# Optimization experiments

Measured on AMD Instinct MI355X. Metric: run time of the kernel, lower is better.

The kernel has to match this reference:

```python
import jax, jax.numpy as jnp
import numpy as np

IN_F = 128
OUT_F = 64


def _xavier(key, shape, gain=1.414):
    fan_in, fan_out = shape[0], shape[1]
    bound = gain * np.sqrt(6.0 / (fan_in + fan_out))
    return jax.random.uniform(key, shape, jnp.float32, -bound, bound)


def setup_inputs() -> dict:
    key = jax.random.key(0)
    ks = jax.random.split(key, 11)
    features = jax.random.normal(ks[0], (2, 32, 2048, IN_F), dtype=jnp.float32)
    d = {"features": features}
    for i in range(4):
        d[f"W{i+1}"] = _xavier(ks[1 + 2 * i], (IN_F, 2 * OUT_F))
        d[f"a{i+1}"] = _xavier(ks[2 + 2 * i], (2 * OUT_F, 1))
    d["Wo"] = _xavier(ks[9], (8 * OUT_F, OUT_F))
    return d


def _head(features, W, a):
    # features: [b,g,n,i]; W: [i,j]; a: [j,1]
    Wx = jnp.einsum('bgni,ij->bgnj', features, W)          # [b,g,n,2F]
    att = jax.nn.softmax(Wx @ a, axis=2)                   # softmax over nodes, [b,g,n,1]
    return jnp.einsum('bgno,bgnj->bgj', att, Wx)           # pooled [b,g,2F]


def reference(features, W1, a1, W2, a2, W3, a3, W4, a4, Wo):
    h1 = _head(features, W1, a1)
    h2 = _head(features, W2, a2)
    h3 = _head(features, W3, a3)
    h4 = _head(features, W4, a4)
    multi = jnp.concatenate([h1, h2, h3, h4], axis=2)      # [b,g,8F]
    return jax.nn.elu(multi @ Wo)                          # [b,g,F]
```

## Files before the change

### kernel.cpp

```cpp
#include <hip/hip_runtime.h>
#include <math.h>

#define BG     64
#define NN     2048
#define F      128
#define OUTF   64
#define NSLICE 32
#define SNODES 64

#define OFF_WEFF 0
#define OFF_FP   512
#define OFF_LP   (512 + BG * NSLICE * 4 * F)

__global__ __launch_bounds__(256) void k_weff(
    const float* __restrict__ W1, const float* __restrict__ a1,
    const float* __restrict__ W2, const float* __restrict__ a2,
    const float* __restrict__ W3, const float* __restrict__ a3,
    const float* __restrict__ W4, const float* __restrict__ a4,
    float* __restrict__ ws) {
  int h = blockIdx.x, t = threadIdx.x;
  const float* W = (h == 0) ? W1 : (h == 1) ? W2 : (h == 2) ? W3 : W4;
  const float* a = (h == 0) ? a1 : (h == 1) ? a2 : (h == 2) ? a3 : a4;
  __shared__ float aL[F];
  __shared__ float part[F][33];

  if (t < F) aL[t] = a[t];
  __syncthreads();

  int c = t & 31, r8 = t >> 5;
#pragma unroll
  for (int it = 0; it < 16; ++it) {
    int row = it * 8 + r8;
    float4 w = ((const float4*)(W + row * F))[c];
    part[row][c] = w.x * aL[4 * c] + w.y * aL[4 * c + 1] +
                   w.z * aL[4 * c + 2] + w.w * aL[4 * c + 3];
  }
  __syncthreads();

  if (t < F) {
    float s = 0.f;
#pragma unroll
    for (int c2 = 0; c2 < 32; ++c2) s += part[t][c2];
    ws[OFF_WEFF + h * F + t] = s;
  }
}

__global__ __launch_bounds__(256) void k_main(
    const float* __restrict__ feat, float* __restrict__ ws) {
  int g = blockIdx.x >> 5;
  int slice = blockIdx.x & (NSLICE - 1);
  int t = threadIdx.x;

  __shared__ float4 sfeat[SNODES * 32];
  __shared__ float4 weffL[4 * 32];
  __shared__ float eLf[SNODES * 4];
  __shared__ float4 pacc[4][2][32];
  __shared__ float sePf[2][4];

  if (t < 128) weffL[t] = ((const float4*)(ws + OFF_WEFF))[t];

  const float4* fb =
      (const float4*)(feat + ((size_t)g * NN + slice * SNODES) * F);
  float4 ld[8];
#pragma unroll
  for (int k = 0; k < 8; ++k) ld[k] = fb[k * 256 + t];
#pragma unroll
  for (int k = 0; k < 8; ++k) {
    int j = k * 256 + t;
    int n = j >> 5, c = j & 31;
    sfeat[n * 32 + (c ^ (n & 31))] = ld[k];
  }
  __syncthreads();

  {
    int n = t & 63, h = t >> 6;
    int sw = n & 31, base = n * 32, wb = h * 32;
    float p = 0.f;
#pragma unroll 8
    for (int c = 0; c < 32; ++c) {
      float4 f = sfeat[base + (c ^ sw)];
      float4 w = weffL[wb + c];
      p += f.x * w.x + f.y * w.y + f.z * w.z + f.w * w.w;
    }
    eLf[n * 4 + h] = __expf(p);
  }
  __syncthreads();

  {
    int i4 = t & 31, q = (t >> 5) & 1, h = t >> 6;
    float4 a0 = make_float4(0.f, 0.f, 0.f, 0.f);
    float se = 0.f;
#pragma unroll 8
    for (int nn = 0; nn < 32; ++nn) {
      int n = q * 32 + nn;
      float4 f = sfeat[n * 32 + (i4 ^ (n & 31))];
      float e = eLf[n * 4 + h];
      a0.x += e * f.x; a0.y += e * f.y; a0.z += e * f.z; a0.w += e * f.w;
      se += e;
    }
    pacc[h][q][i4] = a0;
    if (i4 == 0) sePf[q][h] = se;
  }
  __syncthreads();

  if (t < 128) {
    int i4 = t & 31, h = t >> 5;
    float4 s0 = pacc[h][0][i4], s1 = pacc[h][1][i4];
    float4 s = make_float4(s0.x + s1.x, s0.y + s1.y,
                           s0.z + s1.z, s0.w + s1.w);
    ((float4*)(ws + OFF_FP))[(size_t)(g * NSLICE + slice) * 128 + h * 32 + i4] = s;
  }
  if (t == 0) {
    float4 L = make_float4(sePf[0][0] + sePf[1][0], sePf[0][1] + sePf[1][1],
                           sePf[0][2] + sePf[1][2], sePf[0][3] + sePf[1][3]);
    ((float4*)(ws + OFF_LP))[g * NSLICE + slice] = L;
  }
}

__global__ __launch_bounds__(512) void k_final(
    const float* __restrict__ W1, const float* __restrict__ W2,
    const float* __restrict__ W3, const float* __restrict__ W4,
    const float* __restrict__ Wo, const float* __restrict__ ws,
    float* __restrict__ out) {
  int g = blockIdx.x;
  int t = threadIdx.x;
  __shared__ float fp[512];
  __shared__ float multi[512];
  __shared__ float invl[4];
  __shared__ float part[8][64];

  if (t < 4) {
    float s = 0.f;
#pragma unroll
    for (int sl = 0; sl < NSLICE; ++sl)
      s += ws[OFF_LP + (g * NSLICE + sl) * 4 + t];
    invl[t] = 1.0f / s;
  }
  float s = 0.f;
  const float* fpb = ws + OFF_FP + (size_t)g * NSLICE * 512 + t;
#pragma unroll
  for (int sl = 0; sl < NSLICE; ++sl) s += fpb[sl * 512];
  __syncthreads();
  fp[t] = s * invl[t >> 7];
  __syncthreads();

  int h = t >> 7, col = t & 127;
  const float* W = (h == 0) ? W1 : (h == 1) ? W2 : (h == 2) ? W3 : W4;
  const float* fph = fp + h * F;
  float acc = 0.f;
#pragma unroll 16
  for (int i = 0; i < F; ++i) acc += fph[i] * W[i * F + col];
  multi[t] = acc;
  __syncthreads();

  int o = t & 63, chunk = t >> 6;
  const float* mk = multi + chunk * 64;
  const float* wk = Wo + (size_t)chunk * 64 * OUTF + o;
  float p = 0.f;
#pragma unroll 16
  for (int k = 0; k < 64; ++k) p += mk[k] * wk[k * OUTF];
  part[chunk][o] = p;
  __syncthreads();

  if (t < 64) {
    float acc2 = 0.f;
#pragma unroll
    for (int c = 0; c < 8; ++c) acc2 += part[c][t];
    out[g * OUTF + t] = (acc2 > 0.f) ? acc2 : expm1f(acc2);
  }
}

extern "C" void kernel_launch(void* const* d_in, const int* in_sizes, int n_in,
                              void* d_out, int out_size, void* d_ws, size_t ws_size,
                              hipStream_t stream) {
  const float* feat = (const float*)d_in[0];
  const float* W1 = (const float*)d_in[1];
  const float* a1 = (const float*)d_in[2];
  const float* W2 = (const float*)d_in[3];
  const float* a2 = (const float*)d_in[4];
  const float* W3 = (const float*)d_in[5];
  const float* a3 = (const float*)d_in[6];
  const float* W4 = (const float*)d_in[7];
  const float* a4 = (const float*)d_in[8];
  const float* Wo = (const float*)d_in[9];
  float* ws = (float*)d_ws;
  float* out = (float*)d_out;

  k_weff<<<4, 256, 0, stream>>>(W1, a1, W2, a2, W3, a3, W4, a4, ws);
  k_main<<<BG * NSLICE, 256, 0, stream>>>(feat, ws);
  k_final<<<BG, 512, 0, stream>>>(W1, W2, W3, W4, Wo, ws, out);
}
```

Measured before the change: 119.2 us.

## Fuse final projection into main kernel via last-block atomic counter

Removes the separate k_final launch. Each k_main block bumps an atomic counter for its graph, and the last slice block to finish does the cross-slice reduction, the per-head W projection and the Wo projection with ELU. The final stage now uses float4 weight loads and split-K partial sums held in reused shared memory. This saves a kernel launch and its dependency gap, at the cost of threadfences, an atomic per block, and a serialized tail done by 64 blocks of 256 threads. It also sets launch_bounds occupancy to 4 blocks per SIMD-group.

```diff
diff --git a/kernel.cpp b/kernel.cpp
--- a/kernel.cpp
+++ b/kernel.cpp
@@ -9,8 +9,9 @@
 #define SNODES 64
 
 #define OFF_WEFF 0
-#define OFF_FP   512
-#define OFF_LP   (512 + BG * NSLICE * 4 * F)
+#define OFF_CNT  512
+#define OFF_FP   576
+#define OFF_LP   (576 + BG * NSLICE * 4 * F)
 
 __global__ __launch_bounds__(256) void k_weff(
     const float* __restrict__ W1, const float* __restrict__ a1,
@@ -24,6 +25,8 @@
   __shared__ float aL[F];
   __shared__ float part[F][33];
 
+  if (h == 0 && t < BG) ((int*)(ws + OFF_CNT))[t] = 0;
+
   if (t < F) aL[t] = a[t];
   __syncthreads();
 
@@ -45,8 +48,12 @@
   }
 }
 
-__global__ __launch_bounds__(256) void k_main(
-    const float* __restrict__ feat, float* __restrict__ ws) {
+__global__ __launch_bounds__(256, 4) void k_main(
+    const float* __restrict__ feat,
+    const float* __restrict__ W1, const float* __restrict__ W2,
+    const float* __restrict__ W3, const float* __restrict__ W4,
+    const float* __restrict__ Wo,
+    float* __restrict__ ws, float* __restrict__ out) {
   int g = blockIdx.x >> 5;
   int slice = blockIdx.x & (NSLICE - 1);
   int t = threadIdx.x;
@@ -56,6 +63,7 @@
   __shared__ float eLf[SNODES * 4];
   __shared__ float4 pacc[4][2][32];
   __shared__ float sePf[2][4];
+  __shared__ int lastFlag;
 
   if (t < 128) weffL[t] = ((const float4*)(ws + OFF_WEFF))[t];
 
@@ -115,58 +123,92 @@
                            sePf[0][2] + sePf[1][2], sePf[0][3] + sePf[1][3]);
     ((float4*)(ws + OFF_LP))[g * NSLICE + slice] = L;
   }
-}
-
-__global__ __launch_bounds__(512) void k_final(
-    const float* __restrict__ W1, const float* __restrict__ W2,
-    const float* __restrict__ W3, const float* __restrict__ W4,
-    const float* __restrict__ Wo, const float* __restrict__ ws,
-    float* __restrict__ out) {
-  int g = blockIdx.x;
-  int t = threadIdx.x;
-  __shared__ float fp[512];
-  __shared__ float multi[512];
-  __shared__ float invl[4];
-  __shared__ float part[8][64];
+
+  __threadfence();
+  __syncthreads();
+  if (t == 0) {
+    int old = atomicAdd((int*)(ws + OFF_CNT) + g, 1);
+    lastFlag = (old == NSLICE - 1) ? 1 : 0;
+  }
+  __syncthreads();
+  if (!lastFlag) return;
+  __threadfence();
+
+  float* fbuf = (float*)sfeat;
+  float4* f4 = (float4*)sfeat;
+  const float4* FP4 = (const float4*)(ws + OFF_FP) + (size_t)g * NSLICE * 128;
 
   if (t < 4) {
     float s = 0.f;
 #pragma unroll
     for (int sl = 0; sl < NSLICE; ++sl)
       s += ws[OFF_LP + (g * NSLICE + sl) * 4 + t];
-    invl[t] = 1.0f / s;
-  }
-  float s = 0.f;
-  const float* fpb = ws + OFF_FP + (size_t)g * NSLICE * 512 + t;
-#pragma unroll
-  for (int sl = 0; sl < NSLICE; ++sl) s += fpb[sl * 512];
-  __syncthreads();
-  fp[t] = s * invl[t >> 7];
-  __syncthreads();
-
-  int h = t >> 7, col = t & 127;
-  const float* W = (h == 0) ? W1 : (h == 1) ? W2 : (h == 2) ? W3 : W4;
-  const float* fph = fp + h * F;
-  float acc = 0.f;
-#pragma unroll 16
-  for (int i = 0; i < F; ++i) acc += fph[i] * W[i * F + col];
-  multi[t] = acc;
-  __syncthreads();
-
-  int o = t & 63, chunk = t >> 6;
-  const float* mk = multi + chunk * 64;
-  const float* wk = Wo + (size_t)chunk * 64 * OUTF + o;
-  float p = 0.f;
-#pragma unroll 16
-  for (int k = 0; k < 64; ++k) p += mk[k] * wk[k * OUTF];
-  part[chunk][o] = p;
-  __syncthreads();
-
-  if (t < 64) {
-    float acc2 = 0.f;
-#pragma unroll
-    for (int c = 0; c < 8; ++c) acc2 += part[c][t];
-    out[g * OUTF + t] = (acc2 > 0.f) ? acc2 : expm1f(acc2);
+    fbuf[8188 + t] = 1.0f / s;
+  }
+  {
+    int j = t & 127, half = t >> 7;
+    float4 s4 = make_float4(0.f, 0.f, 0.f, 0.f);
+#pragma unroll
+    for (int sl = 0; sl < 16; ++sl) {
+      float4 v = FP4[(half * 16 + sl) * 128 + j];
+      s4.x += v.x; s4.y += v.y; s4.z += v.z; s4.w += v.w;
+    }
+    f4[half * 128 + j] = s4;
+  }
+  __syncthreads();
+  if (t < 128) {
+    float4 a = f4[t], b = f4[128 + t];
+    float inv = fbuf[8188 + (t >> 5)];
+    f4[256 + t] = make_float4((a.x + b.x) * inv, (a.y + b.y) * inv,
+                              (a.z + b.z) * inv, (a.w + b.w) * inv);
+  }
+  __syncthreads();
+
+  {
+    int c = t & 31, rg = (t >> 5) & 1, h = t >> 6;
+    const float* Wsel = (h == 0) ? W1 : (h == 1) ? W2 : (h == 2) ? W3 : W4;
+    const float4* W4p = (const float4*)Wsel;
+    const float* fph = fbuf + 1024 + h * F;
+    float4 acc = make_float4(0.f, 0.f, 0.f, 0.f);
+#pragma unroll 8
+    for (int k = 0; k < 64; ++k) {
+      int i = rg * 64 + k;
+      float s = fph[i];
+      float4 w = W4p[i * 32 + c];
+      acc.x += s * w.x; acc.y += s * w.y; acc.z += s * w.z; acc.w += s * w.w;
+    }
+    f4[512 + (h * 2 + rg) * 32 + c] = acc;
+  }
+  __syncthreads();
+  if (t < 128) {
+    int h = t >> 5, c = t & 31;
+    float4 a = f4[512 + (h * 2) * 32 + c];
+    float4 b = f4[512 + (h * 2 + 1) * 32 + c];
+    f4[768 + h * 32 + c] = make_float4(a.x + b.x, a.y + b.y,
+                                       a.z + b.z, a.w + b.w);
+  }
+  __syncthreads();
+
+  {
+    int o4 = t & 15, rg = t >> 4;
+    const float4* Wo4 = (const float4*)Wo;
+    const float* mu = fbuf + 3072;
+    float4 acc = make_float4(0.f, 0.f, 0.f, 0.f);
+#pragma unroll 8
+    for (int k = 0; k < 32; ++k) {
+      int i = rg * 32 + k;
+      float s = mu[i];
+      float4 w = Wo4[i * 16 + o4];
+      acc.x += s * w.x; acc.y += s * w.y; acc.z += s * w.z; acc.w += s * w.w;
+    }
+    f4[rg * 16 + o4] = acc;
+  }
+  __syncthreads();
+  if (t < OUTF) {
+    float s = 0.f;
+#pragma unroll
+    for (int rg = 0; rg < 16; ++rg) s += fbuf[rg * 64 + t];
+    out[g * OUTF + t] = (s > 0.f) ? s : expm1f(s);
   }
 }
 
@@ -187,6 +229,5 @@
   float* out = (float*)d_out;
 
   k_weff<<<4, 256, 0, stream>>>(W1, a1, W2, a2, W3, a3, W4, a4, ws);
-  k_main<<<BG * NSLICE, 256, 0, stream>>>(feat, ws);
-  k_final<<<BG, 512, 0, stream>>>(W1, W2, W3, W4, Wo, ws, out);
+  k_main<<<BG * NSLICE, 256, 0, stream>>>(feat, W1, W2, W3, W4, Wo, ws, out);
 }
```

Result: slower. 345.4 us (+189.7%).
